# Optimization experiments

Hardware: AMD Instinct MI355X
Metric: run time of the kernel (lower is better)

Reference implementation:

```python
import jax, jax.numpy as jnp
import numpy as np

B, T, D, H, FF, L = 4, 2048, 512, 8, 2048, 4
IN_SIZE = 32
PAST, FUT = 128, 128
HD = D // H
EPS = 1e-5


def _layer_norm(x, g, b):
    m = jnp.mean(x, axis=-1, keepdims=True)
    v = jnp.mean((x - m) ** 2, axis=-1, keepdims=True)
    return (x - m) / jnp.sqrt(v + EPS) * g + b


def setup_inputs() -> dict:
    key = jax.random.key(0)
    ks = jax.random.split(key, 20)
    s = 0.02
    inp = {
        "beatmap_features": jax.random.normal(ks[0], (B, T, IN_SIZE), jnp.float32),
        "positions": jax.random.normal(ks[1], (B, T, 2), jnp.float32),
        "proj_w": jax.random.normal(ks[2], (D, IN_SIZE), jnp.float32) * s,
        "proj_b": jnp.zeros((D,), jnp.float32),
        "pos_enc": jax.random.normal(ks[3], (T, D), jnp.float32),
        # stacked per-layer params, leading dim L
        "qkv_w": jax.random.normal(ks[4], (L, 3 * D, D), jnp.float32) * s,
        "qkv_b": jnp.zeros((L, 3 * D), jnp.float32),
        "out_w": jax.random.normal(ks[5], (L, D, D), jnp.float32) * s,
        "out_b": jnp.zeros((L, D), jnp.float32),
        "ff1_w": jax.random.normal(ks[6], (L, FF, D), jnp.float32) * s,
        "ff1_b": jnp.zeros((L, FF), jnp.float32),
        "ff2_w": jax.random.normal(ks[7], (L, D, FF), jnp.float32) * s,
        "ff2_b": jnp.zeros((L, D), jnp.float32),
        "ln1_g": jnp.ones((L, D), jnp.float32),
        "ln1_b": jnp.zeros((L, D), jnp.float32),
        "ln2_g": jnp.ones((L, D), jnp.float32),
        "ln2_b": jnp.zeros((L, D), jnp.float32),
    }
    return inp


def reference(beatmap_features, positions, proj_w, proj_b, pos_enc,
              qkv_w, qkv_b, out_w, out_b, ff1_w, ff1_b, ff2_w, ff2_b,
              ln1_g, ln1_b, ln2_g, ln2_b):
    # positions only perturbed by noise during training; eval forward ignores it.
    x = beatmap_features @ proj_w.T + proj_b + pos_enc[None]  # [B,T,D]

    # banded local-window additive mask: allow j in [i-PAST, i+FUT]
    i = jnp.arange(T)[:, None]
    j = jnp.arange(T)[None, :]
    allow = (j >= i - PAST) & (j <= i + FUT)
    mask = jnp.where(allow, 0.0, -jnp.inf).astype(x.dtype)  # [T,T]

    scale = 1.0 / jnp.sqrt(jnp.asarray(HD, x.dtype))

    def enc_layer(x, p):
        qkvw, qkvb, ow, ob, f1w, f1b, f2w, f2b, g1, b1, g2, b2 = p
        qkv = x @ qkvw.T + qkvb                         # [B,T,3D]
        q, k, v = jnp.split(qkv, 3, axis=-1)
        q = q.reshape(B, T, H, HD).transpose(0, 2, 1, 3)  # [B,H,T,HD]
        k = k.reshape(B, T, H, HD).transpose(0, 2, 1, 3)
        v = v.reshape(B, T, H, HD).transpose(0, 2, 1, 3)
        scores = jnp.einsum('bhqd,bhkd->bhqk', q, k) * scale + mask
        attn = jax.nn.softmax(scores, axis=-1)
        o = jnp.einsum('bhqk,bhkd->bhqd', attn, v)
        o = o.transpose(0, 2, 1, 3).reshape(B, T, D) @ ow.T + ob
        x = _layer_norm(x + o, g1, b1)                  # post-norm (PyTorch default)
        h = jax.nn.relu(x @ f1w.T + f1b) @ f2w.T + f2b
        x = _layer_norm(x + h, g2, b2)
        return x, None

    params = (qkv_w, qkv_b, out_w, out_b, ff1_w, ff1_b, ff2_w, ff2_b,
              ln1_g, ln1_b, ln2_g, ln2_b)
    x, _ = jax.lax.scan(enc_layer, x, params)
    return x
```

## Files before the change

### kernel.cpp

```cpp
#include <hip/hip_runtime.h>
#include <hip/hip_bf16.h>

#define B_ 4
#define T_ 2048
#define D_ 512
#define H_ 8
#define FF_ 2048
#define L_ 4
#define NTOK 8192
#define EPS_ 1e-5f

typedef __hip_bfloat16 bf16;
typedef __attribute__((ext_vector_type(8))) short short8;
typedef __attribute__((ext_vector_type(4))) float floatx4;

__device__ __forceinline__ float bf2f(short s) {
    union { unsigned u; float f; } cv;
    cv.u = ((unsigned)(unsigned short)s) << 16;
    return cv.f;
}
__device__ __forceinline__ short f2bs(float f) {
    union { bf16 b; short s; } cv;
    cv.b = __float2bfloat16(f);
    return cv.s;
}

__global__ __launch_bounds__(256) void cvt_kernel(
    const float* __restrict__ in, bf16* __restrict__ out, int n4)
{
    int i = blockIdx.x * 256 + threadIdx.x;
    if (i >= n4) return;
    float4 v = ((const float4*)in)[i];
    out[i * 4 + 0] = __float2bfloat16(v.x);
    out[i * 4 + 1] = __float2bfloat16(v.y);
    out[i * 4 + 2] = __float2bfloat16(v.z);
    out[i * 4 + 3] = __float2bfloat16(v.w);
}

__global__ __launch_bounds__(256) void transpose_pw(
    const float* __restrict__ pw, float* __restrict__ pwT)
{
    int idx = blockIdx.x * 256 + threadIdx.x;
    int d = idx >> 5, k = idx & 31;
    pwT[k * D_ + d] = pw[idx];
}

__global__ __launch_bounds__(256) void proj_kernel(
    const float* __restrict__ feat, const float* __restrict__ pwT,
    const float* __restrict__ pb, const float* __restrict__ pe,
    float* __restrict__ x, bf16* __restrict__ xb)
{
    __shared__ float fs[16][32];
    int tok0 = blockIdx.x * 16;
    int tid = threadIdx.x;
    {
        float2 v = ((const float2*)(feat + (size_t)tok0 * 32))[tid];
        fs[tid >> 4][(tid & 15) * 2]     = v.x;
        fs[tid >> 4][(tid & 15) * 2 + 1] = v.y;
    }
    int d0 = tid * 2;
    float w0[32], w1[32];
    #pragma unroll
    for (int k = 0; k < 32; k++) {
        float2 wv = *(const float2*)(pwT + k * D_ + d0);
        w0[k] = wv.x; w1[k] = wv.y;
    }
    float2 pbv = *(const float2*)(pb + d0);
    __syncthreads();
    #pragma unroll 4
    for (int tok = 0; tok < 16; tok++) {
        int t = (tok0 + tok) & (T_ - 1);
        float s0 = pbv.x, s1 = pbv.y;
        #pragma unroll
        for (int k = 0; k < 32; k++) {
            float f = fs[tok][k];
            s0 += f * w0[k]; s1 += f * w1[k];
        }
        float2 pev = *(const float2*)(pe + (size_t)t * D_ + d0);
        s0 += pev.x; s1 += pev.y;
        size_t o = (size_t)(tok0 + tok) * D_ + d0;
        *(float2*)(x + o) = make_float2(s0, s1);
        union { struct { short a, b; } s; unsigned u; } pk;
        pk.s.a = f2bs(s0); pk.s.b = f2bs(s1);
        *(unsigned*)((short*)xb + o) = pk.u;
    }
}

template <int RELU>
__global__ __launch_bounds__(256) void gemm_bf16_kernel(
    const short* __restrict__ A, const short* __restrict__ W,
    const float* __restrict__ bias, bf16* __restrict__ Cb,
    int M, int N, int K)
{
    __shared__ __align__(16) short lds[128 * 136];
    int bm = blockIdx.y * 128, bn = blockIdx.x * 128;
    int tid = threadIdx.x;
    int w = tid >> 6, lane = tid & 63;
    int wm = (w >> 1) * 64, wn = (w & 1) * 64;

    floatx4 acc[4][4];
    #pragma unroll
    for (int i = 0; i < 4; i++)
        #pragma unroll
        for (int j = 0; j < 4; j++)
            acc[i][j] = (floatx4){0.f, 0.f, 0.f, 0.f};

    int r0 = tid >> 2;
    int c0 = tid & 3;
    int slot = (c0 ^ ((r0 >> 1) & 3)) * 8;
    const short* Arow0 = A + (size_t)(bm + r0) * K + c0 * 8;
    const short* Arow1 = A + (size_t)(bm + r0 + 64) * K + c0 * 8;
    const short* Brow0 = W + (size_t)(bn + r0) * K + c0 * 8;
    const short* Brow1 = W + (size_t)(bn + r0 + 64) * K + c0 * 8;

    int lrow = lane & 15, lk = lane >> 4;

    short8 ea0, ea1, eb0, eb1;
    short8 oa0, oa1, ob0, ob1;
    ea0 = *(const short8*)(Arow0);       ea1 = *(const short8*)(Arow1);
    eb0 = *(const short8*)(Brow0);       eb1 = *(const short8*)(Brow1);
    oa0 = *(const short8*)(Arow0 + 32);  oa1 = *(const short8*)(Arow1 + 32);
    ob0 = *(const short8*)(Brow0 + 32);  ob1 = *(const short8*)(Brow1 + 32);

    int nIter = K >> 5;
    for (int it = 0; it < nIter; it += 2) {
        #pragma unroll
        for (int half = 0; half < 2; half++) {
            short* As = lds + half * 8192;
            short* Bs = lds + half * 8192 + 4096;
            if (half == 0) {
                *(short8*)&As[r0 * 32 + slot] = ea0;
                *(short8*)&As[(r0 + 64) * 32 + slot] = ea1;
                *(short8*)&Bs[r0 * 32 + slot] = eb0;
                *(short8*)&Bs[(r0 + 64) * 32 + slot] = eb1;
            } else {
                *(short8*)&As[r0 * 32 + slot] = oa0;
                *(short8*)&As[(r0 + 64) * 32 + slot] = oa1;
                *(short8*)&Bs[r0 * 32 + slot] = ob0;
                *(short8*)&Bs[(r0 + 64) * 32 + slot] = ob1;
            }
            __syncthreads();
            int kn = (it + half + 2) * 32;
            if (kn < K) {
                if (half == 0) {
                    ea0 = *(const short8*)(Arow0 + kn);
                    ea1 = *(const short8*)(Arow1 + kn);
                    eb0 = *(const short8*)(Brow0 + kn);
                    eb1 = *(const short8*)(Brow1 + kn);
                } else {
                    oa0 = *(const short8*)(Arow0 + kn);
                    oa1 = *(const short8*)(Arow1 + kn);
                    ob0 = *(const short8*)(Brow0 + kn);
                    ob1 = *(const short8*)(Brow1 + kn);
                }
            }
            short8 af[4], bfr[4];
            #pragma unroll
            for (int i = 0; i < 4; i++) {
                int rr = wm + i * 16 + lrow;
                af[i] = *(const short8*)&As[rr * 32 + ((lk ^ ((rr >> 1) & 3)) * 8)];
                int nn = wn + i * 16 + lrow;
                bfr[i] = *(const short8*)&Bs[nn * 32 + ((lk ^ ((nn >> 1) & 3)) * 8)];
            }
            #pragma unroll
            for (int i = 0; i < 4; i++)
                #pragma unroll
                for (int j = 0; j < 4; j++)
                    acc[i][j] = __builtin_amdgcn_mfma_f32_16x16x32_bf16(
                        af[i], bfr[j], acc[i][j], 0, 0, 0);
        }
    }

    __syncthreads();

    int cl = lane & 15, rq = lane >> 4;
    #pragma unroll
    for (int i = 0; i < 4; i++) {
        #pragma unroll
        for (int j = 0; j < 4; j++) {
            int col = wn + j * 16 + cl;
            float bv = bias[bn + col];
            #pragma unroll
            for (int r = 0; r < 4; r++) {
                int row = wm + i * 16 + rq * 4 + r;
                float v = acc[i][j][r] + bv;
                if (RELU) v = fmaxf(v, 0.f);
                lds[row * 136 + col] = f2bs(v);
            }
        }
    }
    __syncthreads();

    #pragma unroll
    for (int s = 0; s < 8; s++) {
        int idx = tid + 256 * s;
        int r = idx >> 4, c8 = (idx & 15) * 8;
        short8 v = *(const short8*)&lds[r * 136 + c8];
        *(short8*)((short*)Cb + (size_t)(bm + r) * N + bn + c8) = v;
    }
}

__global__ __launch_bounds__(256, 4) void attn_kernel(
    const short* __restrict__ qkv, bf16* __restrict__ out)
{
    __shared__ __align__(16) short Qs[64 * 72];
    __shared__ __align__(16) short Ks[64 * 72];
    __shared__ __align__(16) short Vt[64 * 72];
    __shared__ __align__(16) short Ps[64 * 72];

    int q0 = blockIdx.x * 64;
    int bh = blockIdx.y;
    int b = bh >> 3, h = bh & 7;
    int tid = threadIdx.x;
    int w = tid >> 6, lane = tid & 63;
    int col = lane & 15, quad = lane >> 4;

    const size_t base = (size_t)b * T_ * 3 * D_;
    const int roww = 3 * D_;
    const int qoff = h * 64, koff = D_ + h * 64, voff = 2 * D_ + h * 64;

    #pragma unroll
    for (int i = 0; i < 2; i++) {
        int idx = tid + 256 * i;
        int r = idx >> 3, c8 = (idx & 7) * 8;
        *(short8*)&Qs[r * 72 + c8] =
            *(const short8*)(qkv + base + (size_t)(q0 + r) * roww + qoff + c8);
    }

    float l_r[4] = {0.f, 0.f, 0.f, 0.f};
    floatx4 Oacc[4];
    #pragma unroll
    for (int j = 0; j < 4; j++) Oacc[j] = (floatx4){0.f, 0.f, 0.f, 0.f};

    int klo = max(0, q0 - 128), khi = min(T_, q0 + 192);
    const float scale = 0.125f;
    int qrow = q0 + w * 16 + quad * 4;

    for (int kt = klo; kt < khi; kt += 64) {
        __syncthreads();
        #pragma unroll
        for (int i = 0; i < 2; i++) {
            int idx = tid + 256 * i;
            int r = idx >> 3, c8 = (idx & 7) * 8;
            *(short8*)&Ks[r * 72 + c8] =
                *(const short8*)(qkv + base + (size_t)(kt + r) * roww + koff + c8);
            short8 v = *(const short8*)(qkv + base + (size_t)(kt + r) * roww + voff + c8);
            #pragma unroll
            for (int u = 0; u < 8; u++) Vt[(c8 + u) * 72 + r] = v[u];
        }
        __syncthreads();

        short8 aq0 = *(const short8*)&Qs[(w * 16 + col) * 72 + quad * 8];
        short8 aq1 = *(const short8*)&Qs[(w * 16 + col) * 72 + 32 + quad * 8];
        floatx4 Sacc[4];
        #pragma unroll
        for (int j = 0; j < 4; j++) {
            short8 bk0 = *(const short8*)&Ks[(j * 16 + col) * 72 + quad * 8];
            short8 bk1 = *(const short8*)&Ks[(j * 16 + col) * 72 + 32 + quad * 8];
            floatx4 s = (floatx4){0.f, 0.f, 0.f, 0.f};
            s = __builtin_amdgcn_mfma_f32_16x16x32_bf16(aq0, bk0, s, 0, 0, 0);
            s = __builtin_amdgcn_mfma_f32_16x16x32_bf16(aq1, bk1, s, 0, 0, 0);
            Sacc[j] = s;
        }

        float ps[4] = {0.f, 0.f, 0.f, 0.f};
        #pragma unroll
        for (int j = 0; j < 4; j++) {
            int key = kt + j * 16 + col;
            #pragma unroll
            for (int r = 0; r < 4; r++) {
                int dj = key - (qrow + r);
                float p = (dj < -128 || dj > 128) ? 0.f : __expf(Sacc[j][r] * scale);
                ps[r] += p;
                Ps[(w * 16 + quad * 4 + r) * 72 + j * 16 + col] = f2bs(p);
            }
        }
        #pragma unroll
        for (int off = 1; off < 16; off <<= 1)
            #pragma unroll
            for (int r = 0; r < 4; r++)
                ps[r] += __shfl_xor(ps[r], off);
        #pragma unroll
        for (int r = 0; r < 4; r++) l_r[r] += ps[r];

        __syncthreads();

        short8 ap0 = *(const short8*)&Ps[(w * 16 + col) * 72 + quad * 8];
        short8 ap1 = *(const short8*)&Ps[(w * 16 + col) * 72 + 32 + quad * 8];
        #pragma unroll
        for (int j = 0; j < 4; j++) {
            short8 bv0 = *(const short8*)&Vt[(j * 16 + col) * 72 + quad * 8];
            short8 bv1 = *(const short8*)&Vt[(j * 16 + col) * 72 + 32 + quad * 8];
            Oacc[j] = __builtin_amdgcn_mfma_f32_16x16x32_bf16(ap0, bv0, Oacc[j], 0, 0, 0);
            Oacc[j] = __builtin_amdgcn_mfma_f32_16x16x32_bf16(ap1, bv1, Oacc[j], 0, 0, 0);
        }
    }

    float invl[4];
    #pragma unroll
    for (int r = 0; r < 4; r++) invl[r] = 1.0f / l_r[r];
    #pragma unroll
    for (int j = 0; j < 4; j++)
        #pragma unroll
        for (int r = 0; r < 4; r++)
            out[(size_t)(b * T_ + qrow + r) * D_ + h * 64 + j * 16 + col] =
                __float2bfloat16(Oacc[j][r] * invl[r]);
}

__global__ __launch_bounds__(256) void add_ln_kernel(
    const float* __restrict__ x, const short* __restrict__ delta,
    const float* __restrict__ g, const float* __restrict__ bta,
    float* __restrict__ out, bf16* __restrict__ outb)
{
    int wave = threadIdx.x >> 6, lane = threadIdx.x & 63;
    int row = blockIdx.x * 4 + wave;
    int c0 = lane * 8;
    const float* xr = x + (size_t)row * D_ + c0;
    float4 xa = *(const float4*)xr;
    float4 xc = *(const float4*)(xr + 4);
    short8 db = *(const short8*)(delta + (size_t)row * D_ + c0);
    float v[8];
    v[0] = xa.x + bf2f(db[0]); v[1] = xa.y + bf2f(db[1]);
    v[2] = xa.z + bf2f(db[2]); v[3] = xa.w + bf2f(db[3]);
    v[4] = xc.x + bf2f(db[4]); v[5] = xc.y + bf2f(db[5]);
    v[6] = xc.z + bf2f(db[6]); v[7] = xc.w + bf2f(db[7]);
    float s = 0.f;
    #pragma unroll
    for (int i = 0; i < 8; i++) s += v[i];
    #pragma unroll
    for (int off = 32; off > 0; off >>= 1) s += __shfl_xor(s, off);
    float mean = s * (1.0f / D_);
    float var = 0.f;
    #pragma unroll
    for (int i = 0; i < 8; i++) { float c = v[i] - mean; var += c * c; }
    #pragma unroll
    for (int off = 32; off > 0; off >>= 1) var += __shfl_xor(var, off);
    float inv = rsqrtf(var * (1.0f / D_) + EPS_);
    float4 g0 = *(const float4*)(g + c0), g1 = *(const float4*)(g + c0 + 4);
    float4 b0 = *(const float4*)(bta + c0), b1 = *(const float4*)(bta + c0 + 4);
    float o[8];
    o[0] = (v[0] - mean) * inv * g0.x + b0.x;
    o[1] = (v[1] - mean) * inv * g0.y + b0.y;
    o[2] = (v[2] - mean) * inv * g0.z + b0.z;
    o[3] = (v[3] - mean) * inv * g0.w + b0.w;
    o[4] = (v[4] - mean) * inv * g1.x + b1.x;
    o[5] = (v[5] - mean) * inv * g1.y + b1.y;
    o[6] = (v[6] - mean) * inv * g1.z + b1.z;
    o[7] = (v[7] - mean) * inv * g1.w + b1.w;
    float* orow = out + (size_t)row * D_ + c0;
    *(float4*)orow = make_float4(o[0], o[1], o[2], o[3]);
    *(float4*)(orow + 4) = make_float4(o[4], o[5], o[6], o[7]);
    short8 ob;
    #pragma unroll
    for (int i = 0; i < 8; i++) ob[i] = f2bs(o[i]);
    *(short8*)((short*)outb + (size_t)row * D_ + c0) = ob;
}

extern "C" void kernel_launch(void* const* d_in, const int* in_sizes, int n_in,
                              void* d_out, int out_size, void* d_ws, size_t ws_size,
                              hipStream_t stream)
{
    const float* feat    = (const float*)d_in[0];
    const float* proj_w  = (const float*)d_in[2];
    const float* proj_b  = (const float*)d_in[3];
    const float* pos_enc = (const float*)d_in[4];
    const float* qkv_w   = (const float*)d_in[5];
    const float* qkv_b   = (const float*)d_in[6];
    const float* out_w   = (const float*)d_in[7];
    const float* out_b   = (const float*)d_in[8];
    const float* ff1_w   = (const float*)d_in[9];
    const float* ff1_b   = (const float*)d_in[10];
    const float* ff2_w   = (const float*)d_in[11];
    const float* ff2_b   = (const float*)d_in[12];
    const float* ln1_g   = (const float*)d_in[13];
    const float* ln1_b   = (const float*)d_in[14];
    const float* ln2_g   = (const float*)d_in[15];
    const float* ln2_b   = (const float*)d_in[16];

    char* p = (char*)d_ws;
    float* x    = (float*)p;  p += (size_t)NTOK * D_ * 4;
    float* pwT  = (float*)p;  p += (size_t)32 * D_ * 4;
    bf16* tmp2b = (bf16*)p;   p += (size_t)NTOK * D_ * 2;
    bf16* xb    = (bf16*)p;   p += (size_t)NTOK * D_ * 2;
    bf16* qkvb  = (bf16*)p;   p += (size_t)NTOK * 3 * D_ * 2;
    bf16* hbuf  = (bf16*)p;   p += (size_t)NTOK * FF_ * 2;
    bf16* abuf  = (bf16*)p;   p += (size_t)NTOK * D_ * 2;
    bf16* wq    = (bf16*)p;   p += (size_t)L_ * 3 * D_ * D_ * 2;
    bf16* wo    = (bf16*)p;   p += (size_t)L_ * D_ * D_ * 2;
    bf16* w1    = (bf16*)p;   p += (size_t)L_ * FF_ * D_ * 2;
    bf16* w2    = (bf16*)p;   p += (size_t)L_ * D_ * FF_ * 2;
    float* outp = (float*)d_out;

    {
        int n4;
        n4 = L_ * 3 * D_ * D_ / 4; cvt_kernel<<<(n4 + 255) / 256, 256, 0, stream>>>(qkv_w, wq, n4);
        n4 = L_ * D_ * D_ / 4;     cvt_kernel<<<(n4 + 255) / 256, 256, 0, stream>>>(out_w, wo, n4);
        n4 = L_ * FF_ * D_ / 4;    cvt_kernel<<<(n4 + 255) / 256, 256, 0, stream>>>(ff1_w, w1, n4);
        n4 = L_ * D_ * FF_ / 4;    cvt_kernel<<<(n4 + 255) / 256, 256, 0, stream>>>(ff2_w, w2, n4);
        transpose_pw<<<64, 256, 0, stream>>>(proj_w, pwT);
    }

    proj_kernel<<<NTOK / 16, 256, 0, stream>>>(feat, pwT, proj_b, pos_enc, x, xb);

    for (int l = 0; l < L_; l++) {
        gemm_bf16_kernel<0><<<dim3(3 * D_ / 128, NTOK / 128), 256, 0, stream>>>(
            (const short*)xb, (const short*)(wq + (size_t)l * 3 * D_ * D_),
            qkv_b + (size_t)l * 3 * D_, qkvb, NTOK, 3 * D_, D_);
        attn_kernel<<<dim3(T_ / 64, B_ * H_), 256, 0, stream>>>((const short*)qkvb, abuf);
        gemm_bf16_kernel<0><<<dim3(D_ / 128, NTOK / 128), 256, 0, stream>>>(
            (const short*)abuf, (const short*)(wo + (size_t)l * D_ * D_),
            out_b + (size_t)l * D_, tmp2b, NTOK, D_, D_);
        add_ln_kernel<<<NTOK / 4, 256, 0, stream>>>(
            x, (const short*)tmp2b, ln1_g + (size_t)l * D_, ln1_b + (size_t)l * D_, x, xb);
        gemm_bf16_kernel<1><<<dim3(FF_ / 128, NTOK / 128), 256, 0, stream>>>(
            (const short*)xb, (const short*)(w1 + (size_t)l * FF_ * D_),
            ff1_b + (size_t)l * FF_, hbuf, NTOK, FF_, D_);
        gemm_bf16_kernel<0><<<dim3(D_ / 128, NTOK / 128), 256, 0, stream>>>(
            (const short*)hbuf, (const short*)(w2 + (size_t)l * D_ * FF_),
            ff2_b + (size_t)l * D_, tmp2b, NTOK, D_, FF_);
        float* dst = (l == L_ - 1) ? outp : x;
        add_ln_kernel<<<NTOK / 4, 256, 0, stream>>>(
            x, (const short*)tmp2b, ln2_g + (size_t)l * D_, ln2_b + (size_t)l * D_, dst, xb);
    }
}
```

Baseline: 680.7 us.

## Split-K narrow GEMMs, drop fp32 residual stream, merge weight prep kernels

```diff
diff --git a/kernel.cpp b/kernel.cpp
--- a/kernel.cpp
+++ b/kernel.cpp
@@ -25,30 +25,35 @@
     return cv.s;
 }
 
-__global__ __launch_bounds__(256) void cvt_kernel(
-    const float* __restrict__ in, bf16* __restrict__ out, int n4)
-{
-    int i = blockIdx.x * 256 + threadIdx.x;
-    if (i >= n4) return;
-    float4 v = ((const float4*)in)[i];
-    out[i * 4 + 0] = __float2bfloat16(v.x);
-    out[i * 4 + 1] = __float2bfloat16(v.y);
-    out[i * 4 + 2] = __float2bfloat16(v.z);
-    out[i * 4 + 3] = __float2bfloat16(v.w);
-}
-
-__global__ __launch_bounds__(256) void transpose_pw(
-    const float* __restrict__ pw, float* __restrict__ pwT)
-{
-    int idx = blockIdx.x * 256 + threadIdx.x;
-    int d = idx >> 5, k = idx & 31;
-    pwT[k * D_ + d] = pw[idx];
+__global__ __launch_bounds__(256) void prep_kernel(
+    const float* __restrict__ s0, const float* __restrict__ s1,
+    const float* __restrict__ s2, const float* __restrict__ s3,
+    bf16* __restrict__ dst, const float* __restrict__ pw, float* __restrict__ pwT)
+{
+    int bid = blockIdx.x;
+    if (bid >= 12288) {
+        int idx = (bid - 12288) * 256 + threadIdx.x;
+        int d = idx >> 5, k = idx & 31;
+        pwT[k * D_ + d] = pw[idx];
+        return;
+    }
+    long i = (long)bid * 256 + threadIdx.x;
+    const float* src; long off;
+    if (i < 786432)       { src = s0; off = i; }
+    else if (i < 1048576) { src = s1; off = i - 786432; }
+    else if (i < 2097152) { src = s2; off = i - 1048576; }
+    else                  { src = s3; off = i - 2097152; }
+    float4 v = ((const float4*)src)[off];
+    union { short s[4]; uint2 u; } pk;
+    pk.s[0] = f2bs(v.x); pk.s[1] = f2bs(v.y);
+    pk.s[2] = f2bs(v.z); pk.s[3] = f2bs(v.w);
+    *(uint2*)((short*)dst + i * 4) = pk.u;
 }
 
 __global__ __launch_bounds__(256) void proj_kernel(
     const float* __restrict__ feat, const float* __restrict__ pwT,
     const float* __restrict__ pb, const float* __restrict__ pe,
-    float* __restrict__ x, bf16* __restrict__ xb)
+    bf16* __restrict__ xb)
 {
     __shared__ float fs[16][32];
     int tok0 = blockIdx.x * 16;
@@ -79,7 +84,6 @@
         float2 pev = *(const float2*)(pe + (size_t)t * D_ + d0);
         s0 += pev.x; s1 += pev.y;
         size_t o = (size_t)(tok0 + tok) * D_ + d0;
-        *(float2*)(x + o) = make_float2(s0, s1);
         union { struct { short a, b; } s; unsigned u; } pk;
         pk.s.a = f2bs(s0); pk.s.b = f2bs(s1);
         *(unsigned*)((short*)xb + o) = pk.u;
@@ -90,10 +94,11 @@
 __global__ __launch_bounds__(256) void gemm_bf16_kernel(
     const short* __restrict__ A, const short* __restrict__ W,
     const float* __restrict__ bias, bf16* __restrict__ Cb,
-    int M, int N, int K)
+    int M, int N, int Kstride, int Kloc)
 {
     __shared__ __align__(16) short lds[128 * 136];
     int bm = blockIdx.y * 128, bn = blockIdx.x * 128;
+    int kbase = blockIdx.z * Kloc;
     int tid = threadIdx.x;
     int w = tid >> 6, lane = tid & 63;
     int wm = (w >> 1) * 64, wn = (w & 1) * 64;
@@ -108,10 +113,10 @@
     int r0 = tid >> 2;
     int c0 = tid & 3;
     int slot = (c0 ^ ((r0 >> 1) & 3)) * 8;
-    const short* Arow0 = A + (size_t)(bm + r0) * K + c0 * 8;
-    const short* Arow1 = A + (size_t)(bm + r0 + 64) * K + c0 * 8;
-    const short* Brow0 = W + (size_t)(bn + r0) * K + c0 * 8;
-    const short* Brow1 = W + (size_t)(bn + r0 + 64) * K + c0 * 8;
+    const short* Arow0 = A + (size_t)(bm + r0) * Kstride + kbase + c0 * 8;
+    const short* Arow1 = A + (size_t)(bm + r0 + 64) * Kstride + kbase + c0 * 8;
+    const short* Brow0 = W + (size_t)(bn + r0) * Kstride + kbase + c0 * 8;
+    const short* Brow1 = W + (size_t)(bn + r0 + 64) * Kstride + kbase + c0 * 8;
 
     int lrow = lane & 15, lk = lane >> 4;
 
@@ -122,7 +127,7 @@
     oa0 = *(const short8*)(Arow0 + 32);  oa1 = *(const short8*)(Arow1 + 32);
     ob0 = *(const short8*)(Brow0 + 32);  ob1 = *(const short8*)(Brow1 + 32);
 
-    int nIter = K >> 5;
+    int nIter = Kloc >> 5;
     for (int it = 0; it < nIter; it += 2) {
         #pragma unroll
         for (int half = 0; half < 2; half++) {
@@ -141,7 +146,7 @@
             }
             __syncthreads();
             int kn = (it + half + 2) * 32;
-            if (kn < K) {
+            if (kn < Kloc) {
                 if (half == 0) {
                     ea0 = *(const short8*)(Arow0 + kn);
                     ea1 = *(const short8*)(Arow1 + kn);
@@ -174,12 +179,13 @@
     __syncthreads();
 
     int cl = lane & 15, rq = lane >> 4;
+    bool z0 = (blockIdx.z == 0);
     #pragma unroll
     for (int i = 0; i < 4; i++) {
         #pragma unroll
         for (int j = 0; j < 4; j++) {
             int col = wn + j * 16 + cl;
-            float bv = bias[bn + col];
+            float bv = z0 ? bias[bn + col] : 0.f;
             #pragma unroll
             for (int r = 0; r < 4; r++) {
                 int row = wm + i * 16 + rq * 4 + r;
@@ -191,12 +197,13 @@
     }
     __syncthreads();
 
+    bf16* Cz = Cb + (size_t)blockIdx.z * M * N;
     #pragma unroll
     for (int s = 0; s < 8; s++) {
         int idx = tid + 256 * s;
         int r = idx >> 4, c8 = (idx & 15) * 8;
         short8 v = *(const short8*)&lds[r * 136 + c8];
-        *(short8*)((short*)Cb + (size_t)(bm + r) * N + bn + c8) = v;
+        *(short8*)((short*)Cz + (size_t)(bm + r) * N + bn + c8) = v;
     }
 }
 
@@ -308,25 +315,25 @@
 }
 
 __global__ __launch_bounds__(256) void add_ln_kernel(
-    const float* __restrict__ x, const short* __restrict__ delta,
+    const short* __restrict__ xb, const short* __restrict__ d0,
+    const short* __restrict__ d1,
     const float* __restrict__ g, const float* __restrict__ bta,
-    float* __restrict__ out, bf16* __restrict__ outb)
+    bf16* __restrict__ outb, float* __restrict__ outf)
 {
     int wave = threadIdx.x >> 6, lane = threadIdx.x & 63;
     int row = blockIdx.x * 4 + wave;
     int c0 = lane * 8;
-    const float* xr = x + (size_t)row * D_ + c0;
-    float4 xa = *(const float4*)xr;
-    float4 xc = *(const float4*)(xr + 4);
-    short8 db = *(const short8*)(delta + (size_t)row * D_ + c0);
+    size_t o = (size_t)row * D_ + c0;
+    short8 xv = *(const short8*)(xb + o);
+    short8 a0 = *(const short8*)(d0 + o);
+    short8 a1 = *(const short8*)(d1 + o);
     float v[8];
-    v[0] = xa.x + bf2f(db[0]); v[1] = xa.y + bf2f(db[1]);
-    v[2] = xa.z + bf2f(db[2]); v[3] = xa.w + bf2f(db[3]);
-    v[4] = xc.x + bf2f(db[4]); v[5] = xc.y + bf2f(db[5]);
-    v[6] = xc.z + bf2f(db[6]); v[7] = xc.w + bf2f(db[7]);
     float s = 0.f;
     #pragma unroll
-    for (int i = 0; i < 8; i++) s += v[i];
+    for (int i = 0; i < 8; i++) {
+        v[i] = bf2f(xv[i]) + bf2f(a0[i]) + bf2f(a1[i]);
+        s += v[i];
+    }
     #pragma unroll
     for (int off = 32; off > 0; off >>= 1) s += __shfl_xor(s, off);
     float mean = s * (1.0f / D_);
@@ -338,22 +345,23 @@
     float inv = rsqrtf(var * (1.0f / D_) + EPS_);
     float4 g0 = *(const float4*)(g + c0), g1 = *(const float4*)(g + c0 + 4);
     float4 b0 = *(const float4*)(bta + c0), b1 = *(const float4*)(bta + c0 + 4);
-    float o[8];
-    o[0] = (v[0] - mean) * inv * g0.x + b0.x;
-    o[1] = (v[1] - mean) * inv * g0.y + b0.y;
-    o[2] = (v[2] - mean) * inv * g0.z + b0.z;
-    o[3] = (v[3] - mean) * inv * g0.w + b0.w;
-    o[4] = (v[4] - mean) * inv * g1.x + b1.x;
-    o[5] = (v[5] - mean) * inv * g1.y + b1.y;
-    o[6] = (v[6] - mean) * inv * g1.z + b1.z;
-    o[7] = (v[7] - mean) * inv * g1.w + b1.w;
-    float* orow = out + (size_t)row * D_ + c0;
-    *(float4*)orow = make_float4(o[0], o[1], o[2], o[3]);
-    *(float4*)(orow + 4) = make_float4(o[4], o[5], o[6], o[7]);
+    float ov[8];
+    ov[0] = (v[0] - mean) * inv * g0.x + b0.x;
+    ov[1] = (v[1] - mean) * inv * g0.y + b0.y;
+    ov[2] = (v[2] - mean) * inv * g0.z + b0.z;
+    ov[3] = (v[3] - mean) * inv * g0.w + b0.w;
+    ov[4] = (v[4] - mean) * inv * g1.x + b1.x;
+    ov[5] = (v[5] - mean) * inv * g1.y + b1.y;
+    ov[6] = (v[6] - mean) * inv * g1.z + b1.z;
+    ov[7] = (v[7] - mean) * inv * g1.w + b1.w;
     short8 ob;
     #pragma unroll
-    for (int i = 0; i < 8; i++) ob[i] = f2bs(o[i]);
-    *(short8*)((short*)outb + (size_t)row * D_ + c0) = ob;
+    for (int i = 0; i < 8; i++) ob[i] = f2bs(ov[i]);
+    *(short8*)((short*)outb + o) = ob;
+    if (outf) {
+        *(float4*)(outf + o) = make_float4(ov[0], ov[1], ov[2], ov[3]);
+        *(float4*)(outf + o + 4) = make_float4(ov[4], ov[5], ov[6], ov[7]);
+    }
 }
 
 extern "C" void kernel_launch(void* const* d_in, const int* in_sizes, int n_in,
@@ -378,10 +386,9 @@
     const float* ln2_b   = (const float*)d_in[16];
 
     char* p = (char*)d_ws;
-    float* x    = (float*)p;  p += (size_t)NTOK * D_ * 4;
     float* pwT  = (float*)p;  p += (size_t)32 * D_ * 4;
-    bf16* tmp2b = (bf16*)p;   p += (size_t)NTOK * D_ * 2;
     bf16* xb    = (bf16*)p;   p += (size_t)NTOK * D_ * 2;
+    bf16* dpar  = (bf16*)p;   p += (size_t)2 * NTOK * D_ * 2;
     bf16* qkvb  = (bf16*)p;   p += (size_t)NTOK * 3 * D_ * 2;
     bf16* hbuf  = (bf16*)p;   p += (size_t)NTOK * FF_ * 2;
     bf16* abuf  = (bf16*)p;   p += (size_t)NTOK * D_ * 2;
@@ -391,35 +398,31 @@
     bf16* w2    = (bf16*)p;   p += (size_t)L_ * D_ * FF_ * 2;
     float* outp = (float*)d_out;
 
-    {
-        int n4;
-        n4 = L_ * 3 * D_ * D_ / 4; cvt_kernel<<<(n4 + 255) / 256, 256, 0, stream>>>(qkv_w, wq, n4);
-        n4 = L_ * D_ * D_ / 4;     cvt_kernel<<<(n4 + 255) / 256, 256, 0, stream>>>(out_w, wo, n4);
-        n4 = L_ * FF_ * D_ / 4;    cvt_kernel<<<(n4 + 255) / 256, 256, 0, stream>>>(ff1_w, w1, n4);
-        n4 = L_ * D_ * FF_ / 4;    cvt_kernel<<<(n4 + 255) / 256, 256, 0, stream>>>(ff2_w, w2, n4);
-        transpose_pw<<<64, 256, 0, stream>>>(proj_w, pwT);
-    }
-
-    proj_kernel<<<NTOK / 16, 256, 0, stream>>>(feat, pwT, proj_b, pos_enc, x, xb);
+    prep_kernel<<<12288 + 64, 256, 0, stream>>>(
+        qkv_w, out_w, ff1_w, ff2_w, wq, proj_w, pwT);
+
+    proj_kernel<<<NTOK / 16, 256, 0, stream>>>(feat, pwT, proj_b, pos_enc, xb);
 
     for (int l = 0; l < L_; l++) {
-        gemm_bf16_kernel<0><<<dim3(3 * D_ / 128, NTOK / 128), 256, 0, stream>>>(
+        gemm_bf16_kernel<0><<<dim3(3 * D_ / 128, NTOK / 128, 1), 256, 0, stream>>>(
             (const short*)xb, (const short*)(wq + (size_t)l * 3 * D_ * D_),
-            qkv_b + (size_t)l * 3 * D_, qkvb, NTOK, 3 * D_, D_);
+            qkv_b + (size_t)l * 3 * D_, qkvb, NTOK, 3 * D_, D_, D_);
         attn_kernel<<<dim3(T_ / 64, B_ * H_), 256, 0, stream>>>((const short*)qkvb, abuf);
-        gemm_bf16_kernel<0><<<dim3(D_ / 128, NTOK / 128), 256, 0, stream>>>(
+        gemm_bf16_kernel<0><<<dim3(D_ / 128, NTOK / 128, 2), 256, 0, stream>>>(
             (const short*)abuf, (const short*)(wo + (size_t)l * D_ * D_),
-            out_b + (size_t)l * D_, tmp2b, NTOK, D_, D_);
+            out_b + (size_t)l * D_, dpar, NTOK, D_, D_, D_ / 2);
         add_ln_kernel<<<NTOK / 4, 256, 0, stream>>>(
-            x, (const short*)tmp2b, ln1_g + (size_t)l * D_, ln1_b + (size_t)l * D_, x, xb);
-        gemm_bf16_kernel<1><<<dim3(FF_ / 128, NTOK / 128), 256, 0, stream>>>(
+            (const short*)xb, (const short*)dpar, (const short*)(dpar + (size_t)NTOK * D_),
+            ln1_g + (size_t)l * D_, ln1_b + (size_t)l * D_, xb, nullptr);
+        gemm_bf16_kernel<1><<<dim3(FF_ / 128, NTOK / 128, 1), 256, 0, stream>>>(
             (const short*)xb, (const short*)(w1 + (size_t)l * FF_ * D_),
-            ff1_b + (size_t)l * FF_, hbuf, NTOK, FF_, D_);
-        gemm_bf16_kernel<0><<<dim3(D_ / 128, NTOK / 128), 256, 0, stream>>>(
+            ff1_b + (size_t)l * FF_, hbuf, NTOK, FF_, D_, D_);
+        gemm_bf16_kernel<0><<<dim3(D_ / 128, NTOK / 128, 2), 256, 0, stream>>>(
             (const short*)hbuf, (const short*)(w2 + (size_t)l * D_ * FF_),
-            ff2_b + (size_t)l * D_, tmp2b, NTOK, D_, FF_);
-        float* dst = (l == L_ - 1) ? outp : x;
+            ff2_b + (size_t)l * D_, dpar, NTOK, D_, FF_, FF_ / 2);
+        float* dst = (l == L_ - 1) ? outp : nullptr;
         add_ln_kernel<<<NTOK / 4, 256, 0, stream>>>(
-            x, (const short*)tmp2b, ln2_g + (size_t)l * D_, ln2_b + (size_t)l * D_, dst, xb);
-    }
-}
+            (const short*)xb, (const short*)dpar, (const short*)(dpar + (size_t)NTOK * D_),
+            ln2_g + (size_t)l * D_, ln2_b + (size_t)l * D_, xb, dst);
+    }
+}
```

Result: faster. 660.0 us (-3.0%).
